# Performance work log

Hardware: AMD Instinct MI355X
Metric: run time of the kernel (lower is better)

## Reference

```python
import jax, jax.numpy as jnp
import numpy as np


def setup_inputs() -> dict:
    key = jax.random.key(0)
    B, U, I, H = 8192, 16, 128, 128
    k = jax.random.split(key, 6)
    s = 1.0 / np.sqrt(H)  # PyTorch GRU init scale (uniform(-s, s)); use scaled normal for test data
    return {
        "inputs": jax.random.normal(k[0], (B, U, I), dtype=jnp.float32),
        "hidden": jax.random.normal(k[1], (B, U, H), dtype=jnp.float32),
        "w_ih": jax.random.normal(k[2], (U, 3 * H, I), dtype=jnp.float32) * s,
        "w_hh": jax.random.normal(k[3], (U, 3 * H, H), dtype=jnp.float32) * s,
        "b_ih": jax.random.normal(k[4], (U, 3 * H), dtype=jnp.float32) * s,
        "b_hh": jax.random.normal(k[5], (U, 3 * H), dtype=jnp.float32) * s,
    }


def reference(inputs, hidden, w_ih, w_hh, b_ih, b_hh):
    # Grouped single-step GRU: one independent GRU cell per unit u, batched via einsum.
    # PyTorch GRU gate order in the 3H dim: [reset, update, new].
    H = hidden.shape[-1]
    # gates_x[b,u,g] = sum_i inputs[b,u,i] * w_ih[u,g,i] + b_ih[u,g]
    gx = jnp.einsum("bui,ugi->bug", inputs, w_ih) + b_ih  # (B, U, 3H)
    gh = jnp.einsum("buh,ugh->bug", hidden, w_hh) + b_hh  # (B, U, 3H)
    xr, xz, xn = gx[..., :H], gx[..., H:2 * H], gx[..., 2 * H:]
    hr, hz, hn = gh[..., :H], gh[..., H:2 * H], gh[..., 2 * H:]
    r = jax.nn.sigmoid(xr + hr)
    z = jax.nn.sigmoid(xz + hz)
    n = jnp.tanh(xn + r * hn)
    return (1.0 - z) * n + z * hidden  # (B, U, H)
```

## Files before the change

kernel.cpp:

```cpp
#include <hip/hip_runtime.h>
#include <hip/hip_bf16.h>

typedef __attribute__((ext_vector_type(8))) short  short8;
typedef __attribute__((ext_vector_type(4))) float  floatx4;

#define TM   64
#define UH   2048
#define XPAD 264

#define MFMA16(a,b,c) __builtin_amdgcn_mfma_f32_16x16x32_bf16(a, b, c, 0, 0, 0)

__global__ __launch_bounds__(256) void prep(const float* __restrict__ w_ih,
                                            const float* __restrict__ w_hh,
                                            const float* __restrict__ b_ih,
                                            const float* __restrict__ b_hh,
                                            __hip_bfloat16* __restrict__ Wc,
                                            float* __restrict__ bias_c) {
    if (blockIdx.x < 1536) {
        int idx = blockIdx.x * 256 + threadIdx.x;
        int row = idx >> 6;
        int k   = (idx & 63) * 4;
        const float* src = (k < 128) ? (w_ih + (size_t)row * 128 + k)
                                     : (w_hh + (size_t)row * 128 + (k - 128));
        float4 v = *(const float4*)src;
        __hip_bfloat16* d = Wc + (size_t)row * 256 + k;
        d[0] = __float2bfloat16(v.x);
        d[1] = __float2bfloat16(v.y);
        d[2] = __float2bfloat16(v.z);
        d[3] = __float2bfloat16(v.w);
    } else {
        int idx = (blockIdx.x - 1536) * 256 + threadIdx.x;
        int u = idx >> 9;
        int g = idx & 511;
        float v;
        if (g < 256)       v = b_ih[u * 384 + g] + b_hh[u * 384 + g];
        else if (g < 384)  v = b_ih[u * 384 + g];
        else               v = b_hh[u * 384 + (g - 128)];
        bias_c[idx] = v;
    }
}

__global__ __launch_bounds__(256, 2) void gru_fused(
    const float* __restrict__ inputs, const float* __restrict__ hidden,
    const __hip_bfloat16* __restrict__ Wc, const float* __restrict__ bias_c,
    float* __restrict__ out)
{
    __shared__ __align__(16) __hip_bfloat16 Xs[TM][XPAD];
    __shared__ float bs[512];

    const int bx  = blockIdx.x;
    const int mt  = bx & 127;
    const int u   = bx >> 7;
    const int b0  = mt * TM;
    const int tid = threadIdx.x;

    bs[tid]       = bias_c[u * 512 + tid];
    bs[tid + 256] = bias_c[u * 512 + tid + 256];

    const float* xbase = inputs + (size_t)b0 * UH + u * 128;
    const float* hbase = hidden + (size_t)b0 * UH + u * 128;
    #pragma unroll
    for (int i = 0; i < 16; ++i) {
        int f   = i * 256 + tid;
        int row = f >> 6;
        int col = (f & 63) * 4;
        const float* src = (col < 128) ? (xbase + (size_t)row * UH + col)
                                       : (hbase + (size_t)row * UH + (col - 128));
        float4 v = *(const float4*)src;
        __hip_bfloat16* d = &Xs[row][col];
        d[0] = __float2bfloat16(v.x);
        d[1] = __float2bfloat16(v.y);
        d[2] = __float2bfloat16(v.z);
        d[3] = __float2bfloat16(v.w);
    }
    __syncthreads();

    const int lane = tid & 63;
    const int wv   = tid >> 6;
    const int lr   = lane & 15;
    const int lq   = lane >> 4;

    floatx4 acc[2][4][4];
    #pragma unroll
    for (int ct = 0; ct < 2; ++ct)
        #pragma unroll
        for (int cat = 0; cat < 4; ++cat)
            #pragma unroll
            for (int m4 = 0; m4 < 4; ++m4)
                acc[ct][cat][m4] = (floatx4){0.f, 0.f, 0.f, 0.f};

    const short* Wg = (const short*)(Wc + (size_t)u * 384 * 256);
    const int koff = lq * 8;

    #pragma unroll
    for (int s = 0; s < 8; ++s) {
        short8 aF[4];
        #pragma unroll
        for (int m4 = 0; m4 < 4; ++m4)
            aF[m4] = *(const short8*)((const short*)&Xs[m4 * 16 + lr][0] + s * 32 + koff);

        #pragma unroll
        for (int ct = 0; ct < 2; ++ct) {
            const int gc = wv * 32 + ct * 16 + lr;
            const short* base = Wg + (size_t)gc * 256 + s * 32 + koff;
            short8 bR = *(const short8*)(base);
            short8 bZ = *(const short8*)(base + 128 * 256);
            short8 bN = *(const short8*)(base + 256 * 256);
            #pragma unroll
            for (int m4 = 0; m4 < 4; ++m4) {
                acc[ct][0][m4] = MFMA16(aF[m4], bR, acc[ct][0][m4]);
                acc[ct][1][m4] = MFMA16(aF[m4], bZ, acc[ct][1][m4]);
                if (s < 4) acc[ct][2][m4] = MFMA16(aF[m4], bN, acc[ct][2][m4]);
                else       acc[ct][3][m4] = MFMA16(aF[m4], bN, acc[ct][3][m4]);
            }
        }
    }

    #pragma unroll
    for (int ct = 0; ct < 2; ++ct) {
        const int c = wv * 32 + ct * 16 + lr;
        const float br  = bs[c];
        const float bz  = bs[128 + c];
        const float bxn = bs[256 + c];
        const float bhn = bs[384 + c];
        #pragma unroll
        for (int m4 = 0; m4 < 4; ++m4) {
            #pragma unroll
            for (int r = 0; r < 4; ++r) {
                const int m = m4 * 16 + lq * 4 + r;
                float rv = 1.f / (1.f + __expf(-(acc[ct][0][m4][r] + br)));
                float zv = 1.f / (1.f + __expf(-(acc[ct][1][m4][r] + bz)));
                float npre = (acc[ct][2][m4][r] + bxn) + rv * (acc[ct][3][m4][r] + bhn);
                float e  = __expf(2.f * npre);
                float nv = 1.f - 2.f / (e + 1.f);
                float hv = __bfloat162float(Xs[m][128 + c]);
                out[(size_t)(b0 + m) * UH + u * 128 + c] = (1.f - zv) * nv + zv * hv;
            }
        }
    }
}


extern "C" void kernel_launch(void* const* d_in, const int* in_sizes, int n_in,
                              void* d_out, int out_size, void* d_ws, size_t ws_size,
                              hipStream_t stream) {
    const float* inputs = (const float*)d_in[0];
    const float* hidden = (const float*)d_in[1];
    const float* w_ih   = (const float*)d_in[2];
    const float* w_hh   = (const float*)d_in[3];
    const float* b_ih   = (const float*)d_in[4];
    const float* b_hh   = (const float*)d_in[5];
    float* out = (float*)d_out;

    __hip_bfloat16* Wc = (__hip_bfloat16*)d_ws;
    float* bias_c = (float*)((char*)d_ws + (size_t)16 * 384 * 256 * 2);

    prep<<<dim3(1568), dim3(256), 0, stream>>>(w_ih, w_hh, b_ih, b_hh, Wc, bias_c);
    gru_fused<<<dim3(2048), dim3(256), 0, stream>>>(inputs, hidden, Wc, bias_c, out);
}
```

Before: 233.1 us.

## Pre-swizzle weights into MFMA fragment order and use 512-thread blocks

The prep kernel now writes the bf16 weights in per-lane MFMA fragment order, so each wave reads a contiguous 1KB chunk per gate per k-step instead of strided rows. The main kernel doubles threads per block to 512, giving each wave 16 output columns and fewer accumulators, which lowers register pressure and raises occupancy (launch bounds 512,3). The gate math switches to hardware reciprocal and a sigmoid-based tanh, trading a little precision for fewer instructions. Each wave now reuses its A fragments over fewer MFMAs, so LDS reads per MFMA go up.

```diff
diff --git a/kernel.cpp b/kernel.cpp
--- a/kernel.cpp
+++ b/kernel.cpp
@@ -4,7 +4,6 @@
 typedef __attribute__((ext_vector_type(8))) short  short8;
 typedef __attribute__((ext_vector_type(4))) float  floatx4;
 
-#define TM   64
 #define UH   2048
 #define XPAD 264
 
@@ -16,20 +15,27 @@
                                             const float* __restrict__ b_hh,
                                             __hip_bfloat16* __restrict__ Wc,
                                             float* __restrict__ bias_c) {
-    if (blockIdx.x < 1536) {
-        int idx = blockIdx.x * 256 + threadIdx.x;
-        int row = idx >> 6;
-        int k   = (idx & 63) * 4;
+    if (blockIdx.x < 768) {
+        int t   = blockIdx.x * 256 + threadIdx.x;
+        int u   = t / 12288;
+        int rem = t - u * 12288;
+        int gt   = rem >> 9;
+        int s    = (rem >> 6) & 7;
+        int lane = rem & 63;
+        int g = gt * 16 + (lane & 15);
+        int k = s * 32 + (lane >> 4) * 8;
+        int row = u * 384 + g;
         const float* src = (k < 128) ? (w_ih + (size_t)row * 128 + k)
                                      : (w_hh + (size_t)row * 128 + (k - 128));
-        float4 v = *(const float4*)src;
-        __hip_bfloat16* d = Wc + (size_t)row * 256 + k;
-        d[0] = __float2bfloat16(v.x);
-        d[1] = __float2bfloat16(v.y);
-        d[2] = __float2bfloat16(v.z);
-        d[3] = __float2bfloat16(v.w);
+        float4 v0 = ((const float4*)src)[0];
+        float4 v1 = ((const float4*)src)[1];
+        __hip_bfloat16* d = Wc + (size_t)t * 8;
+        d[0] = __float2bfloat16(v0.x);  d[1] = __float2bfloat16(v0.y);
+        d[2] = __float2bfloat16(v0.z);  d[3] = __float2bfloat16(v0.w);
+        d[4] = __float2bfloat16(v1.x);  d[5] = __float2bfloat16(v1.y);
+        d[6] = __float2bfloat16(v1.z);  d[7] = __float2bfloat16(v1.w);
     } else {
-        int idx = (blockIdx.x - 1536) * 256 + threadIdx.x;
+        int idx = (blockIdx.x - 768) * 256 + threadIdx.x;
         int u = idx >> 9;
         int g = idx & 511;
         float v;
@@ -40,28 +46,27 @@
     }
 }
 
-__global__ __launch_bounds__(256, 2) void gru_fused(
+__global__ __launch_bounds__(512, 3) void gru_fused(
     const float* __restrict__ inputs, const float* __restrict__ hidden,
     const __hip_bfloat16* __restrict__ Wc, const float* __restrict__ bias_c,
     float* __restrict__ out)
 {
-    __shared__ __align__(16) __hip_bfloat16 Xs[TM][XPAD];
+    __shared__ __align__(16) __hip_bfloat16 Xs[64][XPAD];
     __shared__ float bs[512];
 
     const int bx  = blockIdx.x;
     const int mt  = bx & 127;
     const int u   = bx >> 7;
-    const int b0  = mt * TM;
+    const int b0  = mt * 64;
     const int tid = threadIdx.x;
 
-    bs[tid]       = bias_c[u * 512 + tid];
-    bs[tid + 256] = bias_c[u * 512 + tid + 256];
+    bs[tid] = bias_c[u * 512 + tid];
 
     const float* xbase = inputs + (size_t)b0 * UH + u * 128;
     const float* hbase = hidden + (size_t)b0 * UH + u * 128;
     #pragma unroll
-    for (int i = 0; i < 16; ++i) {
-        int f   = i * 256 + tid;
+    for (int i = 0; i < 8; ++i) {
+        int f   = i * 512 + tid;
         int row = f >> 6;
         int col = (f & 63) * 4;
         const float* src = (col < 128) ? (xbase + (size_t)row * UH + col)
@@ -80,62 +85,55 @@
     const int lr   = lane & 15;
     const int lq   = lane >> 4;
 
-    floatx4 acc[2][4][4];
+    floatx4 aR[4], aZ[4], aXN[4], aHN[4];
     #pragma unroll
-    for (int ct = 0; ct < 2; ++ct)
-        #pragma unroll
-        for (int cat = 0; cat < 4; ++cat)
-            #pragma unroll
-            for (int m4 = 0; m4 < 4; ++m4)
-                acc[ct][cat][m4] = (floatx4){0.f, 0.f, 0.f, 0.f};
+    for (int m4 = 0; m4 < 4; ++m4) {
+        aR[m4]  = (floatx4){0.f, 0.f, 0.f, 0.f};
+        aZ[m4]  = (floatx4){0.f, 0.f, 0.f, 0.f};
+        aXN[m4] = (floatx4){0.f, 0.f, 0.f, 0.f};
+        aHN[m4] = (floatx4){0.f, 0.f, 0.f, 0.f};
+    }
 
-    const short* Wg = (const short*)(Wc + (size_t)u * 384 * 256);
-    const int koff = lq * 8;
+    const short* WgU = (const short*)Wc + (size_t)u * 98304 + lane * 8;
 
     #pragma unroll
     for (int s = 0; s < 8; ++s) {
         short8 aF[4];
         #pragma unroll
         for (int m4 = 0; m4 < 4; ++m4)
-            aF[m4] = *(const short8*)((const short*)&Xs[m4 * 16 + lr][0] + s * 32 + koff);
+            aF[m4] = *(const short8*)((const short*)&Xs[m4 * 16 + lr][0] + s * 32 + lq * 8);
+
+        short8 bR = *(const short8*)(WgU + (size_t)(wv * 8 + s) * 512);
+        short8 bZ = *(const short8*)(WgU + (size_t)(64 + wv * 8 + s) * 512);
+        short8 bN = *(const short8*)(WgU + (size_t)(128 + wv * 8 + s) * 512);
 
         #pragma unroll
-        for (int ct = 0; ct < 2; ++ct) {
-            const int gc = wv * 32 + ct * 16 + lr;
-            const short* base = Wg + (size_t)gc * 256 + s * 32 + koff;
-            short8 bR = *(const short8*)(base);
-            short8 bZ = *(const short8*)(base + 128 * 256);
-            short8 bN = *(const short8*)(base + 256 * 256);
-            #pragma unroll
-            for (int m4 = 0; m4 < 4; ++m4) {
-                acc[ct][0][m4] = MFMA16(aF[m4], bR, acc[ct][0][m4]);
-                acc[ct][1][m4] = MFMA16(aF[m4], bZ, acc[ct][1][m4]);
-                if (s < 4) acc[ct][2][m4] = MFMA16(aF[m4], bN, acc[ct][2][m4]);
-                else       acc[ct][3][m4] = MFMA16(aF[m4], bN, acc[ct][3][m4]);
-            }
+        for (int m4 = 0; m4 < 4; ++m4) {
+            aR[m4] = MFMA16(aF[m4], bR, aR[m4]);
+            aZ[m4] = MFMA16(aF[m4], bZ, aZ[m4]);
+            if (s < 4) aXN[m4] = MFMA16(aF[m4], bN, aXN[m4]);
+            else       aHN[m4] = MFMA16(aF[m4], bN, aHN[m4]);
         }
     }
 
+    const int c = wv * 16 + lr;
+    const float br  = bs[c];
+    const float bz  = bs[128 + c];
+    const float bxn = bs[256 + c];
+    const float bhn = bs[384 + c];
+    float* obase = out + (size_t)b0 * UH + u * 128 + c;
+
     #pragma unroll
-    for (int ct = 0; ct < 2; ++ct) {
-        const int c = wv * 32 + ct * 16 + lr;
-        const float br  = bs[c];
-        const float bz  = bs[128 + c];
-        const float bxn = bs[256 + c];
-        const float bhn = bs[384 + c];
+    for (int m4 = 0; m4 < 4; ++m4) {
         #pragma unroll
-        for (int m4 = 0; m4 < 4; ++m4) {
-            #pragma unroll
-            for (int r = 0; r < 4; ++r) {
-                const int m = m4 * 16 + lq * 4 + r;
-                float rv = 1.f / (1.f + __expf(-(acc[ct][0][m4][r] + br)));
-                float zv = 1.f / (1.f + __expf(-(acc[ct][1][m4][r] + bz)));
-                float npre = (acc[ct][2][m4][r] + bxn) + rv * (acc[ct][3][m4][r] + bhn);
-                float e  = __expf(2.f * npre);
-                float nv = 1.f - 2.f / (e + 1.f);
-                float hv = __bfloat162float(Xs[m][128 + c]);
-                out[(size_t)(b0 + m) * UH + u * 128 + c] = (1.f - zv) * nv + zv * hv;
-            }
+        for (int r = 0; r < 4; ++r) {
+            const int m = m4 * 16 + lq * 4 + r;
+            float rv = __builtin_amdgcn_rcpf(1.f + __expf(-(aR[m4][r] + br)));
+            float zv = __builtin_amdgcn_rcpf(1.f + __expf(-(aZ[m4][r] + bz)));
+            float npre = (aXN[m4][r] + bxn) + rv * (aHN[m4][r] + bhn);
+            float nv = 2.f * __builtin_amdgcn_rcpf(1.f + __expf(-2.f * npre)) - 1.f;
+            float hv = __bfloat162float(Xs[m][128 + c]);
+            obase[(size_t)m * UH] = nv + zv * (hv - nv);
         }
     }
 }
@@ -155,6 +153,6 @@
     __hip_bfloat16* Wc = (__hip_bfloat16*)d_ws;
     float* bias_c = (float*)((char*)d_ws + (size_t)16 * 384 * 256 * 2);
 
-    prep<<<dim3(1568), dim3(256), 0, stream>>>(w_ih, w_hh, b_ih, b_hh, Wc, bias_c);
-    gru_fused<<<dim3(2048), dim3(256), 0, stream>>>(inputs, hidden, Wc, bias_c, out);
+    prep<<<dim3(800), dim3(256), 0, stream>>>(w_ih, w_hh, b_ih, b_hh, Wc, bias_c);
+    gru_fused<<<dim3(2048), dim3(512), 0, stream>>>(inputs, hidden, Wc, bias_c, out);
 }
```

New measurement: 204.9 us. 12.1% less time.
